# Kernel optimization log

Hardware: AMD Instinct MI355X
Metric: run time of the kernel (lower is better)

Reference implementation:

```python
import jax, jax.numpy as jnp
import numpy as np

INV_SQRT2 = 0.7071067811865476
EPS = 1e-6


def _ln(x, w, b):
    m = x.mean(-1, keepdims=True)
    v = ((x - m) ** 2).mean(-1, keepdims=True)
    return (x - m) * jax.lax.rsqrt(v + 1e-5) * w + b


def setup_inputs() -> dict:
    key = jax.random.key(0)
    ks = jax.random.split(key, 18)
    B, L, D, H = 4, 2048, 1024, 16
    Dh = D // H
    Nf = L // 2 + 1
    s = 0.02
    inp = {
        "x": jax.random.normal(ks[0], (B, L, D), jnp.float32),
        "Wq": jax.random.normal(ks[1], (D, D), jnp.float32) * s,
        "Wv": jax.random.normal(ks[2], (D, D), jnp.float32) * s,
        "Wo": jax.random.normal(ks[3], (D, D), jnp.float32) * s,
        # gate MLP: LayerNorm(Dh) -> Linear(Dh,4Dh) -> GELU -> Linear(4Dh, 2*Nf)
        "g_ln_w": jnp.ones((Dh,), jnp.float32),
        "g_ln_b": jnp.zeros((Dh,), jnp.float32),
        "g_w1": jax.random.normal(ks[4], (Dh, 4 * Dh), jnp.float32) * s,
        "g_b1": jnp.zeros((4 * Dh,), jnp.float32),
        "g_w2": jax.random.normal(ks[5], (4 * Dh, 2 * Nf), jnp.float32) * s,
        "g_b2": jnp.zeros((2 * Nf,), jnp.float32),
        # shared modReLU bias (1, Nf)
        "mod_bias": jax.random.normal(ks[6], (1, Nf), jnp.float32) * s,
        # wavelet gating MLP: LayerNorm(Dh) -> Linear(Dh,Dh) -> GELU -> Linear(Dh,Dh) -> Sigmoid
        "w_ln_w": jnp.ones((Dh,), jnp.float32),
        "w_ln_b": jnp.zeros((Dh,), jnp.float32),
        "w_w1": jax.random.normal(ks[7], (Dh, Dh), jnp.float32) * s,
        "w_b1": jnp.zeros((Dh,), jnp.float32),
        "w_w2": jax.random.normal(ks[8], (Dh, Dh), jnp.float32) * s,
        "w_b2": jnp.zeros((Dh,), jnp.float32),
    }
    return inp


def _spectre_forward(x, Wq, Wv, Wo, g_ln_w, g_ln_b, g_w1, g_b1, g_w2, g_b2,
                     mod_bias, w_ln_w, w_ln_b, w_w1, w_b1, w_w2, w_b2):
    B, L, D = x.shape
    H = 16
    Dh = D // H
    Nf = L // 2 + 1

    q = (x @ Wq).reshape(B, L, H, Dh).transpose(0, 2, 1, 3)  # (B,H,L,Dh)
    v = (x @ Wv).reshape(B, L, H, Dh).transpose(0, 2, 1, 3)  # (B,H,L,Dh)

    q_mean = q.mean(axis=2)  # (B,H,Dh) global query summary

    # spectral gates from global query
    h = _ln(q_mean, g_ln_w, g_ln_b)
    h = jax.nn.gelu(h @ g_w1 + g_b1, approximate=False)
    gate = h @ g_w2 + g_b2  # (B,H,2*Nf)
    g = jax.lax.complex(gate[..., :Nf], gate[..., Nf:])  # (B,H,Nf)

    # complex modReLU on the gate (toeplitz_bandwidth = 0 -> identity)
    mag = jnp.abs(g)
    g = (jax.nn.relu(mag + mod_bias) / (mag + EPS)).astype(g.dtype) * g

    # frequency-domain mixing of v
    Vf = jnp.fft.rfft(v, axis=2)  # (B,H,Nf,Dh)
    Vf = Vf * g[..., None]
    v_mix = jnp.fft.irfft(Vf, n=L, axis=2).astype(x.dtype)  # (B,H,L,Dh)

    # wavelet refinement (eval mode: never skipped)
    # single-level depthwise Haar along L
    a = jnp.asarray(INV_SQRT2, x.dtype)
    ev, od = v_mix[:, :, 0::2, :], v_mix[:, :, 1::2, :]  # (B,H,L/2,Dh)
    lp = (ev + od) * a
    hp = (od - ev) * a

    wh = _ln(q_mean, w_ln_w, w_ln_b)
    wh = jax.nn.gelu(wh @ w_w1 + w_b1, approximate=False)
    wgate = jax.nn.sigmoid(wh @ w_w2 + w_b2)  # (B,H,Dh)
    lp = lp * wgate[:, :, None, :]
    hp = hp * wgate[:, :, None, :]

    # Haar synthesis (perfect reconstruction when gate == 1)
    rec_ev = (lp - hp) * a
    rec_od = (lp + hp) * a
    recon = jnp.stack([rec_ev, rec_od], axis=3).reshape(B, H, L, Dh)
    v_mix = v_mix + recon

    out = v_mix.transpose(0, 2, 1, 3).reshape(B, L, D) @ Wo
    return out


def reference(x, Wq, Wv, Wo, g_ln_w, g_ln_b, g_w1, g_b1, g_w2, g_b2,
              mod_bias, w_ln_w, w_ln_b, w_w1, w_b1, w_w2, w_b2):
    return _spectre_forward(x, Wq, Wv, Wo, g_ln_w, g_ln_b, g_w1, g_b1, g_w2,
                            g_b2, mod_bias, w_ln_w, w_ln_b, w_w1, w_b1, w_w2,
                            w_b2)
```

## Files before the change

### kernel.cpp

```cpp
#include <hip/hip_runtime.h>
#include <hip/hip_fp16.h>
#include <math.h>

typedef unsigned short u16;
typedef _Float16 f16x8 __attribute__((ext_vector_type(8)));
typedef float f32x4 __attribute__((ext_vector_type(4)));
typedef u16 u16x8 __attribute__((ext_vector_type(8)));

#define B_ 4
#define L_ 2048
#define D_ 1024
#define H_ 16
#define DH 64
#define NF 1025
#define BH (B_*H_)

#define Z_OFF    0
#define G_OFF    4194304
#define WSC_OFF  (G_OFF + 262144)
#define XB_OFF   (WSC_OFF + 4096)
#define PART_OFF (XB_OFF + 4096)
#define H1_OFF   (PART_OFF + 131072)
#define QP_OFF   (H1_OFF + 16384)
#define XHI_OFF  (QP_OFF + 32768)
#define WVH_OFF  (XHI_OFF + 4194304)
#define WOH_OFF  (WVH_OFF + 524288)

__device__ __forceinline__ u16 f2h(float f) {
    __half h = __float2half(f);
    return *reinterpret_cast<u16*>(&h);
}
__device__ __forceinline__ float h2fu(unsigned u) {
    u16 v = (u16)u;
    __half h = *reinterpret_cast<__half*>(&v);
    return __half2float(h);
}

__global__ void k_xbar1h(const float* __restrict__ x, float* __restrict__ part,
                         u16* __restrict__ xhi) {
    int t = threadIdx.x;
    int dblk = blockIdx.x, lc = blockIdx.y, b = blockIdx.z;
    int d = dblk*256 + t;
    size_t rowbase = (size_t)b*L_ + (size_t)lc*64;
    const float* px = x + rowbase*D_ + d;
    u16* ph = xhi + rowbase*D_ + d;
    float s = 0.f;
    #pragma unroll 4
    for (int l = 0; l < 64; ++l) {
        float v = px[(size_t)l*D_];
        s += v;
        ph[(size_t)l*D_] = f2h(v);
    }
    part[(size_t)(b*32 + lc)*D_ + d] = s;
}

__global__ void k_xbar2(const float* __restrict__ part, float* __restrict__ xbar) {
    int id = blockIdx.x*256 + threadIdx.x;
    int b = id >> 10, d = id & 1023;
    float s = 0.f;
    for (int c = 0; c < 32; ++c) s += part[(size_t)(b*32 + c)*D_ + d];
    xbar[id] = s * (1.0f/(float)L_);
}

__global__ void k_qmean1(const float* __restrict__ xbar, const float* __restrict__ Wq,
                         float* __restrict__ qpart) {
    int t = threadIdx.x;
    int dblk = blockIdx.x, b = blockIdx.y, kc = blockIdx.z;
    int d = dblk*256 + t;
    const float* xb = xbar + b*D_ + kc*128;
    const float* wq = Wq + (size_t)(kc*128)*D_ + d;
    float s = 0.f;
    #pragma unroll 8
    for (int k = 0; k < 128; ++k) s += xb[k] * wq[(size_t)k*D_];
    qpart[((size_t)kc*B_ + b)*D_ + d] = s;
}

__global__ void k_gates_a(const float* __restrict__ qpart,
                          const float* __restrict__ g_ln_w, const float* __restrict__ g_ln_b,
                          const float* __restrict__ g_w1,  const float* __restrict__ g_b1,
                          const float* __restrict__ w_ln_w, const float* __restrict__ w_ln_b,
                          const float* __restrict__ w_w1,  const float* __restrict__ w_b1,
                          const float* __restrict__ w_w2,  const float* __restrict__ w_b2,
                          float* __restrict__ h1_out, float* __restrict__ wscale) {
    int bh = blockIdx.x;
    int b = bh >> 4, h = bh & 15;
    int t = threadIdx.x;
    __shared__ float qm[64], hg[64], wh[64], w1o[64];

    if (t < 64) {
        float s = 0.f;
        #pragma unroll
        for (int kc = 0; kc < 8; ++kc)
            s += qpart[((size_t)kc*B_ + b)*D_ + h*64 + t];
        qm[t] = s;
    }
    __syncthreads();

    float m = 0.f;
    #pragma unroll
    for (int k = 0; k < 64; ++k) m += qm[k];
    m *= (1.0f/64.0f);
    float var = 0.f;
    #pragma unroll
    for (int k = 0; k < 64; ++k) { float df = qm[k]-m; var += df*df; }
    var *= (1.0f/64.0f);
    float rs = rsqrtf(var + 1e-5f);
    if (t < 64) {
        float c = (qm[t]-m)*rs;
        hg[t] = c*g_ln_w[t] + g_ln_b[t];
        wh[t] = c*w_ln_w[t] + w_ln_b[t];
    }
    __syncthreads();

    {
        float acc = g_b1[t];
        #pragma unroll 16
        for (int k = 0; k < 64; ++k) acc += hg[k]*g_w1[k*256 + t];
        h1_out[bh*256 + t] = 0.5f*acc*(1.0f + erff(acc*0.70710678118654752f));
    }
    if (t < 64) {
        float acc = w_b1[t];
        #pragma unroll 16
        for (int k = 0; k < 64; ++k) acc += wh[k]*w_w1[k*64 + t];
        w1o[t] = 0.5f*acc*(1.0f + erff(acc*0.70710678118654752f));
    }
    __syncthreads();

    if (t < 64) {
        float acc = w_b2[t];
        #pragma unroll 16
        for (int k = 0; k < 64; ++k) acc += w1o[k]*w_w2[k*64 + t];
        wscale[bh*64 + t] = 1.0f + 1.0f/(1.0f + expf(-acc));
    }
}

__global__ __launch_bounds__(256) void k_gate_g(const float* __restrict__ h1_ws,
                                                const float* __restrict__ g_w2,
                                                const float* __restrict__ g_b2,
                                                const float* __restrict__ mod_bias,
                                                float* __restrict__ G) {
    int bh = blockIdx.y;
    int t = threadIdx.x;
    int w = t >> 6, l = t & 63;
    int f = blockIdx.x*64 + l;
    int fc = f < NF ? f : NF-1;
    __shared__ float h1s[256];
    __shared__ float rre[4][64], rim[4][64];
    h1s[t] = h1_ws[bh*256 + t];
    __syncthreads();

    float re = 0.f, im = 0.f;
    const float* gw = g_w2 + (size_t)(w*64)*2050;
    const float* h1p = h1s + w*64;
    #pragma unroll 8
    for (int k = 0; k < 64; ++k) {
        float hv = h1p[k];
        re += hv * gw[(size_t)k*2050 + fc];
        im += hv * gw[(size_t)k*2050 + NF + fc];
    }
    rre[w][l] = re; rim[w][l] = im;
    __syncthreads();
    if (w == 0 && f < NF) {
        float rr = rre[0][l]+rre[1][l]+rre[2][l]+rre[3][l] + g_b2[f];
        float ii = rim[0][l]+rim[1][l]+rim[2][l]+rim[3][l] + g_b2[NF+f];
        float mag = sqrtf(rr*rr + ii*ii);
        float mult = fmaxf(mag + mod_bias[f], 0.f) / (mag + 1e-6f);
        float s = mult * (1.0f/2048.0f);
        float gr = s*rr, gi = s*ii;
        if (f == 0 || f == 1024) gi = 0.f;
        float* Gb = G + (size_t)bh*4096;
        Gb[2*f]   = gr;
        Gb[2*f+1] = gi;
        if (f >= 1 && f <= 1023) {
            Gb[2*(2048-f)]   = gr;
            Gb[2*(2048-f)+1] = -gi;
        }
    }
}

__global__ void k_wsplit(const float* __restrict__ Wv, const float* __restrict__ Wo,
                         u16* __restrict__ WvH, u16* __restrict__ WoH) {
    const float* W = blockIdx.z ? Wo : Wv;
    u16* TH = blockIdx.z ? WoH : WvH;
    __shared__ float tile[32][33];
    int t = threadIdx.x;
    int n0 = blockIdx.x*32, k0 = blockIdx.y*32;
    #pragma unroll
    for (int i = 0; i < 4; ++i) {
        int k = (t >> 5) + 8*i;
        tile[k][t & 31] = W[(size_t)(k0 + k)*D_ + n0 + (t & 31)];
    }
    __syncthreads();
    int n = t >> 3, kc = (t & 7)*4;
    ushort4 h;
    h.x = f2h(tile[kc+0][n]);
    h.y = f2h(tile[kc+1][n]);
    h.z = f2h(tile[kc+2][n]);
    h.w = f2h(tile[kc+3][n]);
    *(ushort4*)&TH[(size_t)(n0 + n)*D_ + k0 + kc] = h;
}

template<int EPI>
__global__ __launch_bounds__(256) void k_mfma_gemm(const u16* __restrict__ Ahi,
                                                   const u16* __restrict__ Bhi,
                                                   float* __restrict__ C) {
    __shared__ u16 AsH[64*64], BsH[128*64];
    int t = threadIdx.x;
    size_t rowBase = (size_t)blockIdx.x * 64;
    int colBase = blockIdx.y * 128;
    f32x4 acc[2][4] = {};
    int lane = t & 63;
    int wr = (t >> 7) & 1, wc = (t >> 6) & 1;
    int lr = lane & 15, lq = lane >> 4;

    for (int k0 = 0; k0 < 1024; k0 += 64) {
        #pragma unroll
        for (int i = 0; i < 2; ++i) {
            int c = t + i*256;
            int r = c >> 3, cs = c & 7;
            int ko = (cs ^ (r & 7)) << 3;
            __builtin_amdgcn_global_load_lds(
                (const __attribute__((address_space(1))) void*)(Ahi + (rowBase + (size_t)r)*D_ + k0 + ko),
                (__attribute__((address_space(3))) void*)(AsH + c*8), 16, 0, 0);
        }
        #pragma unroll
        for (int i = 0; i < 4; ++i) {
            int c = t + i*256;
            int r = c >> 3, cs = c & 7;
            int ko = (cs ^ (r & 7)) << 3;
            __builtin_amdgcn_global_load_lds(
                (const __attribute__((address_space(1))) void*)(Bhi + ((size_t)colBase + r)*D_ + k0 + ko),
                (__attribute__((address_space(3))) void*)(BsH + c*8), 16, 0, 0);
        }
        __syncthreads();
        #pragma unroll
        for (int ks = 0; ks < 2; ++ks) {
            f16x8 ah[2], bh[4];
            #pragma unroll
            for (int m = 0; m < 2; ++m) {
                int row = wr*32 + m*16 + lr;
                int ch = (ks*4 + lq) ^ (row & 7);
                ah[m] = *(const f16x8*)(AsH + row*64 + ch*8);
            }
            #pragma unroll
            for (int n = 0; n < 4; ++n) {
                int row = wc*64 + n*16 + lr;
                int ch = (ks*4 + lq) ^ (row & 7);
                bh[n] = *(const f16x8*)(BsH + row*64 + ch*8);
            }
            #pragma unroll
            for (int m = 0; m < 2; ++m) {
                #pragma unroll
                for (int n = 0; n < 4; ++n) {
                    acc[m][n] = __builtin_amdgcn_mfma_f32_16x16x32_f16(ah[m], bh[n], acc[m][n], 0, 0, 0);
                }
            }
        }
        __syncthreads();
    }

    int cr = lq * 4, cc = lane & 15;
    if (EPI == 0) {
        u16* Z = (u16*)C;
        #pragma unroll
        for (int m = 0; m < 2; ++m) {
            #pragma unroll
            for (int n = 0; n < 4; ++n) {
                int d = colBase + wc*64 + n*16 + cc;
                int hh = d >> 6, pr = (d >> 1) & 31, p = d & 1;
                #pragma unroll
                for (int r = 0; r < 4; ++r) {
                    size_t gr = rowBase + wr*32 + m*16 + cr + r;
                    int b = (int)(gr >> 11), l = (int)(gr & 2047);
                    Z[(((size_t)((b*16 + hh)*32 + pr))*L_ + l)*2 + p] = f2h(acc[m][n][r]);
                }
            }
        }
    } else {
        #pragma unroll
        for (int m = 0; m < 2; ++m) {
            #pragma unroll
            for (int n = 0; n < 4; ++n) {
                int d = colBase + wc*64 + n*16 + cc;
                #pragma unroll
                for (int r = 0; r < 4; ++r) {
                    size_t gr = rowBase + wr*32 + m*16 + cr + r;
                    C[gr*D_ + d] = acc[m][n][r];
                }
            }
        }
    }
}

__device__ __forceinline__ float2 cmulp(float2 a, float2 b) {
    return make_float2(a.x*b.x - a.y*b.y, a.x*b.y + a.y*b.x);
}
__device__ __forceinline__ float2 cadd(float2 a, float2 b){ return make_float2(a.x+b.x, a.y+b.y); }
__device__ __forceinline__ float2 csub(float2 a, float2 b){ return make_float2(a.x-b.x, a.y-b.y); }
__device__ __forceinline__ float2 cnegi(float2 a){ return make_float2(a.y, -a.x); }
__device__ __forceinline__ float2 cposi(float2 a){ return make_float2(-a.y, a.x); }

#define RH_ 0.70710678118654752f

__device__ __forceinline__ void fwd3(float2* e, float2 w1) {
    float2 tA1 = make_float2((w1.x + w1.y)*RH_, (w1.y - w1.x)*RH_);
    float2 tA2 = cnegi(w1);
    float2 tA3 = make_float2((w1.y - w1.x)*RH_, -(w1.x + w1.y)*RH_);
    float2 a, b, d;
    a=e[0]; b=e[4]; e[0]=cadd(a,b); d=csub(a,b); e[4]=cmulp(d, w1);
    a=e[1]; b=e[5]; e[1]=cadd(a,b); d=csub(a,b); e[5]=cmulp(d, tA1);
    a=e[2]; b=e[6]; e[2]=cadd(a,b); d=csub(a,b); e[6]=cmulp(d, tA2);
    a=e[3]; b=e[7]; e[3]=cadd(a,b); d=csub(a,b); e[7]=cmulp(d, tA3);
    float2 w2 = cmulp(w1,w1); float2 w2n = cnegi(w2);
    a=e[0]; b=e[2]; e[0]=cadd(a,b); d=csub(a,b); e[2]=cmulp(d, w2);
    a=e[1]; b=e[3]; e[1]=cadd(a,b); d=csub(a,b); e[3]=cmulp(d, w2n);
    a=e[4]; b=e[6]; e[4]=cadd(a,b); d=csub(a,b); e[6]=cmulp(d, w2);
    a=e[5]; b=e[7]; e[5]=cadd(a,b); d=csub(a,b); e[7]=cmulp(d, w2n);
    float2 w4 = cmulp(w2,w2);
    a=e[0]; b=e[1]; e[0]=cadd(a,b); d=csub(a,b); e[1]=cmulp(d, w4);
    a=e[2]; b=e[3]; e[2]=cadd(a,b); d=csub(a,b); e[3]=cmulp(d, w4);
    a=e[4]; b=e[5]; e[4]=cadd(a,b); d=csub(a,b); e[5]=cmulp(d, w4);
    a=e[6]; b=e[7]; e[6]=cadd(a,b); d=csub(a,b); e[7]=cmulp(d, w4);
}

__device__ __forceinline__ void inv3(float2* e, float2 b1) {
    float2 b2 = cmulp(b1,b1), b4 = cmulp(b2,b2);
    float2 a, bb;
    bb=cmulp(e[1],b4); a=e[0]; e[0]=cadd(a,bb); e[1]=csub(a,bb);
    bb=cmulp(e[3],b4); a=e[2]; e[2]=cadd(a,bb); e[3]=csub(a,bb);
    bb=cmulp(e[5],b4); a=e[4]; e[4]=cadd(a,bb); e[5]=csub(a,bb);
    bb=cmulp(e[7],b4); a=e[6]; e[6]=cadd(a,bb); e[7]=csub(a,bb);
    float2 b2i = cposi(b2);
    bb=cmulp(e[2],b2);  a=e[0]; e[0]=cadd(a,bb); e[2]=csub(a,bb);
    bb=cmulp(e[3],b2i); a=e[1]; e[1]=cadd(a,bb); e[3]=csub(a,bb);
    bb=cmulp(e[6],b2);  a=e[4]; e[4]=cadd(a,bb); e[6]=csub(a,bb);
    bb=cmulp(e[7],b2i); a=e[5]; e[5]=cadd(a,bb); e[7]=csub(a,bb);
    float2 tB1 = make_float2((b1.x - b1.y)*RH_, (b1.x + b1.y)*RH_);
    float2 tB2 = cposi(b1);
    float2 tB3 = make_float2(-(b1.x + b1.y)*RH_, (b1.x - b1.y)*RH_);
    bb=cmulp(e[4],b1);  a=e[0]; e[0]=cadd(a,bb); e[4]=csub(a,bb);
    bb=cmulp(e[5],tB1); a=e[1]; e[1]=cadd(a,bb); e[5]=csub(a,bb);
    bb=cmulp(e[6],tB2); a=e[2]; e[2]=cadd(a,bb); e[6]=csub(a,bb);
    bb=cmulp(e[7],tB3); a=e[3]; e[3]=cadd(a,bb); e[7]=csub(a,bb);
}

__device__ __forceinline__ void inv2(float2* e, float2 b1) {
    float2 b2 = cmulp(b1,b1);
    float2 a, bb;
    bb=cmulp(e[1],b2); a=e[0]; e[0]=cadd(a,bb); e[1]=csub(a,bb);
    bb=cmulp(e[3],b2); a=e[2]; e[2]=cadd(a,bb); e[3]=csub(a,bb);
    float2 b1i = cposi(b1);
    bb=cmulp(e[2],b1);  a=e[0]; e[0]=cadd(a,bb); e[2]=csub(a,bb);
    bb=cmulp(e[3],b1i); a=e[1]; e[1]=cadd(a,bb); e[3]=csub(a,bb);
}

#define PIDX(i) ((i) + ((i)>>5))

__global__ __launch_bounds__(256, 4) void k_fft(unsigned* __restrict__ z16,
                                                const float* __restrict__ G,
                                                const float* __restrict__ wscale) {
    __shared__ float2 dsh[2112];
    int t = threadIdx.x;
    int row = blockIdx.x;
    int bh = row >> 5, jp = row & 31;
    unsigned* zr = z16 + (size_t)row * L_;
    const float PIO = 3.14159265358979323846f;

    float2 e[8];
    #pragma unroll
    for (int j = 0; j < 8; ++j) {
        unsigned u = zr[t + 256*j];
        e[j] = make_float2(h2fu(u & 0xffffu), h2fu(u >> 16));
    }
    {
        float s_, c_; __sincosf(-(PIO/1024.f)*(float)t, &s_, &c_);
        fwd3(e, make_float2(c_, s_));
    }
    #pragma unroll
    for (int j = 0; j < 8; ++j) { int i = t + 256*j; dsh[PIDX(i)] = e[j]; }
    __syncthreads();

    {
        int q = t >> 5, r = t & 31, base = q*256 + r;
        #pragma unroll
        for (int j = 0; j < 8; ++j) { int i = base + 32*j; e[j] = dsh[PIDX(i)]; }
        float s_, c_; __sincosf(-(PIO/128.f)*(float)r, &s_, &c_);
        fwd3(e, make_float2(c_, s_));
        #pragma unroll
        for (int j = 0; j < 8; ++j) { int i = base + 32*j; dsh[PIDX(i)] = e[j]; }
    }
    __syncthreads();

    {
        int q = t >> 2, r = t & 3, base = q*32 + r;
        #pragma unroll
        for (int j = 0; j < 8; ++j) { int i = base + 4*j; e[j] = dsh[PIDX(i)]; }
        float s_, c_; __sincosf(-(PIO/16.f)*(float)r, &s_, &c_);
        fwd3(e, make_float2(c_, s_));
        #pragma unroll
        for (int j = 0; j < 8; ++j) { int i = base + 4*j; dsh[PIDX(i)] = e[j]; }
    }
    __syncthreads();

    {
        #pragma unroll
        for (int u = 0; u < 8; ++u) { int i = 8*t + u; e[u] = dsh[PIDX(i)]; }
        float2 a, b, d;
        a=e[0]; b=e[2]; e[0]=cadd(a,b); e[2]=csub(a,b);
        a=e[1]; b=e[3]; e[1]=cadd(a,b); d=csub(a,b); e[3]=cnegi(d);
        a=e[4]; b=e[6]; e[4]=cadd(a,b); e[6]=csub(a,b);
        a=e[5]; b=e[7]; e[5]=cadd(a,b); d=csub(a,b); e[7]=cnegi(d);
        a=e[0]; b=e[1]; e[0]=cadd(a,b); e[1]=csub(a,b);
        a=e[2]; b=e[3]; e[2]=cadd(a,b); e[3]=csub(a,b);
        a=e[4]; b=e[5]; e[4]=cadd(a,b); e[5]=csub(a,b);
        a=e[6]; b=e[7]; e[6]=cadd(a,b); e[7]=csub(a,b);
        int flo = (int)(__brev((unsigned)t) >> 24);
        const float2* Gb = (const float2*)(G + (size_t)bh*4096);
        e[0] = cmulp(e[0], Gb[flo + 256*0]);
        e[1] = cmulp(e[1], Gb[flo + 256*4]);
        e[2] = cmulp(e[2], Gb[flo + 256*2]);
        e[3] = cmulp(e[3], Gb[flo + 256*6]);
        e[4] = cmulp(e[4], Gb[flo + 256*1]);
        e[5] = cmulp(e[5], Gb[flo + 256*5]);
        e[6] = cmulp(e[6], Gb[flo + 256*3]);
        e[7] = cmulp(e[7], Gb[flo + 256*7]);
        inv3(e, make_float2(1.f, 0.f));
        #pragma unroll
        for (int u = 0; u < 8; ++u) { int i = 8*t + u; dsh[PIDX(i)] = e[u]; }
    }
    __syncthreads();

    {
        int q = t >> 3, r = t & 7, base = q*64 + r;
        #pragma unroll
        for (int j = 0; j < 8; ++j) { int i = base + 8*j; e[j] = dsh[PIDX(i)]; }
        float s_, c_; __sincosf((PIO/32.f)*(float)r, &s_, &c_);
        inv3(e, make_float2(c_, s_));
        #pragma unroll
        for (int j = 0; j < 8; ++j) { int i = base + 8*j; dsh[PIDX(i)] = e[j]; }
    }
    __syncthreads();

    {
        int q = t >> 6, r = t & 63, base = q*512 + r;
        #pragma unroll
        for (int j = 0; j < 8; ++j) { int i = base + 64*j; e[j] = dsh[PIDX(i)]; }
        float s_, c_; __sincosf((PIO/256.f)*(float)r, &s_, &c_);
        inv3(e, make_float2(c_, s_));
        #pragma unroll
        for (int j = 0; j < 8; ++j) { int i = base + 64*j; dsh[PIDX(i)] = e[j]; }
    }
    __syncthreads();

    {
        #pragma unroll
        for (int j = 0; j < 4; ++j) { int i = t + 512*j; e[j] = dsh[PIDX(i)]; }
        #pragma unroll
        for (int j = 0; j < 4; ++j) { int i = t + 256 + 512*j; e[4+j] = dsh[PIDX(i)]; }
        float s_, c_; __sincosf((PIO/1024.f)*(float)t, &s_, &c_);
        float2 b1 = make_float2(c_, s_);
        inv2(e, b1);
        float2 b1b = make_float2((b1.x - b1.y)*RH_, (b1.x + b1.y)*RH_);
        inv2(e+4, b1b);
        float sc0 = wscale[bh*64 + 2*jp];
        float sc1 = wscale[bh*64 + 2*jp + 1];
        #pragma unroll
        for (int j = 0; j < 4; ++j) {
            unsigned lo = f2h(e[j].x*sc0), hi = f2h(e[j].y*sc1);
            zr[t + 512*j] = lo | (hi << 16);
        }
        #pragma unroll
        for (int j = 0; j < 4; ++j) {
            unsigned lo = f2h(e[4+j].x*sc0), hi = f2h(e[4+j].y*sc1);
            zr[t + 256 + 512*j] = lo | (hi << 16);
        }
    }
}

__global__ void k_vsplit(const unsigned* __restrict__ z16, u16* __restrict__ vhi) {
    int t = threadIdx.x;
    int lt = blockIdx.x, h = blockIdx.y, b = blockIdx.z;
    int l0 = lt*64;
    __shared__ unsigned tile[64][33];
    const unsigned* zb = z16 + (size_t)(b*16 + h)*32*L_;
    int pr = t >> 3, lg = t & 7;
    #pragma unroll
    for (int i = 0; i < 8; ++i) {
        int l = lg*8 + i;
        tile[l][pr] = zb[(size_t)pr*L_ + l0 + l];
    }
    __syncthreads();
    int l = t >> 2, q0 = (t & 3) * 8;
    u16x8 o0, o1;
    #pragma unroll
    for (int i = 0; i < 4; ++i) {
        unsigned u = tile[l][q0+i];
        o0[2*i]   = (u16)(u & 0xffffu);
        o0[2*i+1] = (u16)(u >> 16);
    }
    #pragma unroll
    for (int i = 0; i < 4; ++i) {
        unsigned u = tile[l][q0+4+i];
        o1[2*i]   = (u16)(u & 0xffffu);
        o1[2*i+1] = (u16)(u >> 16);
    }
    size_t base = ((size_t)(b*L_) + l0 + l)*D_ + h*64 + q0*2;
    *(u16x8*)&vhi[base]   = o0;
    *(u16x8*)&vhi[base+8] = o1;
}

extern "C" void kernel_launch(void* const* d_in, const int* in_sizes, int n_in,
                              void* d_out, int out_size, void* d_ws, size_t ws_size,
                              hipStream_t stream) {
    const float* x      = (const float*)d_in[0];
    const float* Wq     = (const float*)d_in[1];
    const float* Wv     = (const float*)d_in[2];
    const float* Wo     = (const float*)d_in[3];
    const float* g_ln_w = (const float*)d_in[4];
    const float* g_ln_b = (const float*)d_in[5];
    const float* g_w1   = (const float*)d_in[6];
    const float* g_b1   = (const float*)d_in[7];
    const float* g_w2   = (const float*)d_in[8];
    const float* g_b2   = (const float*)d_in[9];
    const float* mod_b  = (const float*)d_in[10];
    const float* w_ln_w = (const float*)d_in[11];
    const float* w_ln_b = (const float*)d_in[12];
    const float* w_w1   = (const float*)d_in[13];
    const float* w_b1   = (const float*)d_in[14];
    const float* w_w2   = (const float*)d_in[15];
    const float* w_b2   = (const float*)d_in[16];

    float* ws   = (float*)d_ws;
    unsigned* z16 = (unsigned*)(ws + Z_OFF);
    float* G    = ws + G_OFF;
    float* wsc  = ws + WSC_OFF;
    float* xbar = ws + XB_OFF;
    float* part = ws + PART_OFF;
    float* h1ws = ws + H1_OFF;
    float* qpart= ws + QP_OFF;
    u16* xhi = (u16*)(ws + XHI_OFF);
    u16* WvH = (u16*)(ws + WVH_OFF);
    u16* WoH = (u16*)(ws + WOH_OFF);
    u16* vhi = xhi;
    float* outp = (float*)d_out;

    dim3 gx(4, 32, 4);
    k_xbar1h<<<gx, 256, 0, stream>>>(x, part, xhi);
    k_xbar2<<<16, 256, 0, stream>>>(part, xbar);
    dim3 gq(4, 4, 8);
    k_qmean1<<<gq, 256, 0, stream>>>(xbar, Wq, qpart);
    k_gates_a<<<64, 256, 0, stream>>>(qpart, g_ln_w, g_ln_b, g_w1, g_b1,
                                      w_ln_w, w_ln_b, w_w1, w_b1, w_w2, w_b2,
                                      h1ws, wsc);
    dim3 ggate(17, 64);
    k_gate_g<<<ggate, 256, 0, stream>>>(h1ws, g_w2, g_b2, mod_b, G);
    dim3 gw(32, 32, 2);
    k_wsplit<<<gw, 256, 0, stream>>>(Wv, Wo, WvH, WoH);

    dim3 gg(128, 8);
    k_mfma_gemm<0><<<gg, 256, 0, stream>>>(xhi, WvH, (float*)z16);
    k_fft<<<2048, 256, 0, stream>>>(z16, G, wsc);
    dim3 gv(32, 16, 4);
    k_vsplit<<<gv, 256, 0, stream>>>(z16, vhi);
    k_mfma_gemm<1><<<gg, 256, 0, stream>>>(vhi, WoH, outp);
}
```

Before: 131.7 us.

## Double-buffer first GEMM with direct global-to-LDS async loads

Adds a new kernel for the Wv projection GEMM. It double-buffers the LDS tiles and fills them with global_load_lds, so the next K-tile is fetched while MFMAs run on the current one, and it raises wave priority around the compute section. The aim is to hide global memory latency that the single-buffered loop exposed. In exchange the kernel uses twice the LDS, which may lower occupancy, and the second GEMM is left unchanged apart from losing its template parameter.

```diff
diff --git a/kernel.cpp b/kernel.cpp
--- a/kernel.cpp
+++ b/kernel.cpp
@@ -200,7 +200,101 @@
     *(ushort4*)&TH[(size_t)(n0 + n)*D_ + k0 + kc] = h;
 }
 
-template<int EPI>
+__device__ __forceinline__ void p_stageA(const u16* __restrict__ Ag, size_t rowBase, int k0,
+                                         u16* As, int t) {
+    #pragma unroll
+    for (int i = 0; i < 2; ++i) {
+        int c = t + i*256;
+        int r = c >> 3, cs = c & 7;
+        int ko = (cs ^ (r & 7)) << 3;
+        __builtin_amdgcn_global_load_lds(
+            (const __attribute__((address_space(1))) void*)(Ag + (rowBase + (size_t)r)*D_ + k0 + ko),
+            (__attribute__((address_space(3))) void*)(As + c*8), 16, 0, 0);
+    }
+}
+__device__ __forceinline__ void p_stageB(const u16* __restrict__ Bg, int colBase, int k0,
+                                         u16* Bs, int t) {
+    #pragma unroll
+    for (int i = 0; i < 4; ++i) {
+        int c = t + i*256;
+        int r = c >> 3, cs = c & 7;
+        int ko = (cs ^ (r & 7)) << 3;
+        __builtin_amdgcn_global_load_lds(
+            (const __attribute__((address_space(1))) void*)(Bg + ((size_t)colBase + r)*D_ + k0 + ko),
+            (__attribute__((address_space(3))) void*)(Bs + c*8), 16, 0, 0);
+    }
+}
+
+__global__ __launch_bounds__(256) void k_gemm_pipe(const u16* __restrict__ Ahi,
+                                                   const u16* __restrict__ Bhi,
+                                                   float* __restrict__ C) {
+    __shared__ u16 As[2][64*64], Bs[2][128*64];
+    int t = threadIdx.x;
+    size_t rowBase = (size_t)blockIdx.x * 64;
+    int colBase = blockIdx.y * 128;
+    f32x4 acc[2][4] = {};
+    int lane = t & 63;
+    int wr = (t >> 7) & 1, wc = (t >> 6) & 1;
+    int lr = lane & 15, lq = lane >> 4;
+
+    p_stageA(Ahi, rowBase, 0, As[0], t);
+    p_stageB(Bhi, colBase, 0, Bs[0], t);
+    __syncthreads();
+
+    int cur = 0;
+    for (int step = 0; step < 16; ++step) {
+        if (step < 15) {
+            p_stageA(Ahi, rowBase, (step+1)*64, As[cur^1], t);
+            p_stageB(Bhi, colBase, (step+1)*64, Bs[cur^1], t);
+        }
+        __builtin_amdgcn_sched_barrier(0);
+        __builtin_amdgcn_s_setprio(1);
+        #pragma unroll
+        for (int ks = 0; ks < 2; ++ks) {
+            f16x8 ah[2], bh[4];
+            #pragma unroll
+            for (int m = 0; m < 2; ++m) {
+                int row = wr*32 + m*16 + lr;
+                int ch = (ks*4 + lq) ^ (row & 7);
+                ah[m] = *(const f16x8*)(As[cur] + row*64 + ch*8);
+            }
+            #pragma unroll
+            for (int n = 0; n < 4; ++n) {
+                int row = wc*64 + n*16 + lr;
+                int ch = (ks*4 + lq) ^ (row & 7);
+                bh[n] = *(const f16x8*)(Bs[cur] + row*64 + ch*8);
+            }
+            #pragma unroll
+            for (int m = 0; m < 2; ++m) {
+                #pragma unroll
+                for (int n = 0; n < 4; ++n) {
+                    acc[m][n] = __builtin_amdgcn_mfma_f32_16x16x32_f16(ah[m], bh[n], acc[m][n], 0, 0, 0);
+                }
+            }
+        }
+        __builtin_amdgcn_s_setprio(0);
+        __syncthreads();
+        cur ^= 1;
+    }
+
+    int cr = lq * 4, cc = lane & 15;
+    u16* Z = (u16*)C;
+    #pragma unroll
+    for (int m = 0; m < 2; ++m) {
+        #pragma unroll
+        for (int n = 0; n < 4; ++n) {
+            int d = colBase + wc*64 + n*16 + cc;
+            int hh = d >> 6, pr = (d >> 1) & 31, p = d & 1;
+            #pragma unroll
+            for (int r = 0; r < 4; ++r) {
+                size_t gr = rowBase + wr*32 + m*16 + cr + r;
+                int b = (int)(gr >> 11), l = (int)(gr & 2047);
+                Z[(((size_t)((b*16 + hh)*32 + pr))*L_ + l)*2 + p] = f2h(acc[m][n][r]);
+            }
+        }
+    }
+}
+
 __global__ __launch_bounds__(256) void k_mfma_gemm(const u16* __restrict__ Ahi,
                                                    const u16* __restrict__ Bhi,
                                                    float* __restrict__ C) {
@@ -260,33 +354,15 @@
     }
 
     int cr = lq * 4, cc = lane & 15;
-    if (EPI == 0) {
-        u16* Z = (u16*)C;
-        #pragma unroll
-        for (int m = 0; m < 2; ++m) {
-            #pragma unroll
-            for (int n = 0; n < 4; ++n) {
-                int d = colBase + wc*64 + n*16 + cc;
-                int hh = d >> 6, pr = (d >> 1) & 31, p = d & 1;
-                #pragma unroll
-                for (int r = 0; r < 4; ++r) {
-                    size_t gr = rowBase + wr*32 + m*16 + cr + r;
-                    int b = (int)(gr >> 11), l = (int)(gr & 2047);
-                    Z[(((size_t)((b*16 + hh)*32 + pr))*L_ + l)*2 + p] = f2h(acc[m][n][r]);
-                }
-            }
-        }
-    } else {
-        #pragma unroll
-        for (int m = 0; m < 2; ++m) {
-            #pragma unroll
-            for (int n = 0; n < 4; ++n) {
-                int d = colBase + wc*64 + n*16 + cc;
-                #pragma unroll
-                for (int r = 0; r < 4; ++r) {
-                    size_t gr = rowBase + wr*32 + m*16 + cr + r;
-                    C[gr*D_ + d] = acc[m][n][r];
-                }
+    #pragma unroll
+    for (int m = 0; m < 2; ++m) {
+        #pragma unroll
+        for (int n = 0; n < 4; ++n) {
+            int d = colBase + wc*64 + n*16 + cc;
+            #pragma unroll
+            for (int r = 0; r < 4; ++r) {
+                size_t gr = rowBase + wr*32 + m*16 + cr + r;
+                C[gr*D_ + d] = acc[m][n][r];
             }
         }
     }
@@ -558,9 +634,9 @@
     k_wsplit<<<gw, 256, 0, stream>>>(Wv, Wo, WvH, WoH);
 
     dim3 gg(128, 8);
-    k_mfma_gemm<0><<<gg, 256, 0, stream>>>(xhi, WvH, (float*)z16);
+    k_gemm_pipe<<<gg, 256, 0, stream>>>(xhi, WvH, (float*)z16);
     k_fft<<<2048, 256, 0, stream>>>(z16, G, wsc);
     dim3 gv(32, 16, 4);
     k_vsplit<<<gv, 256, 0, stream>>>(z16, vhi);
-    k_mfma_gemm<1><<<gg, 256, 0, stream>>>(vhi, WoH, outp);
-}
+    k_mfma_gemm<<<gg, 256, 0, stream>>>(vhi, WoH, outp);
+}
```

New measurement: 140.5 us. +6.7%, slower.
